# Performance work log

Hardware: AMD Instinct MI355X
Metric: run time of the kernel (lower is better)

Reference implementation:

```python
import jax, jax.numpy as jnp
import numpy as np
from jax import lax

KERNEL = 2  # kernel_size, forced by the (s3-1, s4-1, s5-1) output reshape


def setup_inputs() -> dict:
    key = jax.random.key(0)
    kx, kw = jax.random.split(key)
    x = jax.random.normal(kx, (4, 16, 32, 32, 32), dtype=jnp.float32)
    w = jax.random.normal(kw, (512, 128), dtype=jnp.float32)  # (d1, d2=C*2^3)
    return {"x": x, "w": w}


def _gaussian_kernel(x, w):
    N, C, D, H, W = x.shape
    d1, d2 = w.shape
    # 3D unfold with kernel 2, stride 1, no padding -> (N, C*8, D-1, H-1, W-1)
    patches = lax.conv_general_dilated_patches(
        x,
        filter_shape=(KERNEL, KERNEL, KERNEL),
        window_strides=(1, 1, 1),
        padding='VALID',
    )
    P = (D - 1) * (H - 1) * (W - 1)
    y = patches.reshape(N, d2, P).transpose(0, 2, 1)  # (N, P, d2)
    # sum((y - w)^2) expanded as ||y||^2 - 2 y.w + ||w||^2 to avoid the
    # (N, P, d1, d2) broadcasted difference tensor.
    y_sq = jnp.sum(y * y, axis=-1, keepdims=True)           # (N, P, 1)
    w_sq = jnp.sum(w * w, axis=-1)                          # (d1,)
    cross = jnp.einsum('npd,kd->npk', y, w)                 # (N, P, d1)
    dist = y_sq - 2.0 * cross + w_sq                        # (N, P, d1)
    out = jnp.exp(-dist)
    return out.transpose(0, 2, 1).reshape(N, d1, D - 1, H - 1, W - 1)


def reference(x, w):
    return _gaussian_kernel(x, w)
```

## Files before the change

kernel.cpp:

```cpp
#include <hip/hip_runtime.h>

typedef unsigned char u8;
typedef float f32x4 __attribute__((ext_vector_type(4)));

#define P_OUT 29791
#define NCH   512

__device__ __forceinline__ unsigned pk4_fp8(float a, float b, float c, float d) {
  int v = __builtin_amdgcn_cvt_pk_fp8_f32(a, b, 0, false);
  v = __builtin_amdgcn_cvt_pk_fp8_f32(c, d, v, true);
  return (unsigned)v;
}

__global__ void wprep_kernel(const float* __restrict__ w,
                             u8* __restrict__ wb, float* __restrict__ wsq) {
  const int tid = threadIdx.x;
  const int g = blockIdx.x * 16 + (tid >> 4);
  const int c = tid & 15;
  const float4* wr = (const float4*)(w + g * 128 + c * 8);
  float4 f0 = wr[0], f1 = wr[1];
  float s = f0.x*f0.x + f0.y*f0.y + f0.z*f0.z + f0.w*f0.w
          + f1.x*f1.x + f1.y*f1.y + f1.z*f1.z + f1.w*f1.w;
#pragma unroll
  for (int m = 1; m < 16; m <<= 1) s += __shfl_xor(s, m, 64);
  uint2 pk;
  pk.x = pk4_fp8(f0.x, f0.y, f0.z, f0.w);
  pk.y = pk4_fp8(f1.x, f1.y, f1.z, f1.w);
  *(uint2*)(wb + g * 128 + c * 8) = pk;
  if (c == 0) wsq[g] = s;
}

#define GLDS(g, l) __builtin_amdgcn_global_load_lds(                         \
    (const __attribute__((address_space(1))) unsigned int*)(g),              \
    (__attribute__((address_space(3))) unsigned int*)(l), 16, 0, 0)

__global__ __launch_bounds__(256, 2)
void gauss_fused_kernel(const float* __restrict__ x,
                        const u8* __restrict__ wb,
                        const float* __restrict__ wsq,
                        float* __restrict__ out) {
  __shared__ __align__(16) u8 Ws[128 * 128];
  __shared__ __align__(16) float Xs[16 * 2 * 5 * 32];

  const int bid = blockIdx.x;
  const int tile = (bid & 7) * 496 + (bid >> 3);
  const unsigned nb = (unsigned)tile / 992u;
  const unsigned rem = (unsigned)tile - nb * 992u;
  const unsigned ct = rem / 248u;
  const unsigned r2 = rem - ct * 248u;
  const unsigned d  = r2 >> 3;
  const unsigned hb = r2 & 7;
  const int h0 = hb * 4;
  const int nh = (h0 + 4 <= 31) ? 4 : (31 - h0);
  const int nrows = nh * 31;
  const int c0 = ct * 128;
  const int tp0 = d * 961 + h0 * 31;

  const int tid = threadIdx.x;
  const int wid = tid >> 6;
  const int lane = tid & 63;
  const int quad = lane >> 4;
  const int col = lane & 15;
  const int wch = wid & 1;
  const int wp = wid >> 1;

#pragma unroll
  for (int t = 0; t < 4; ++t) {
    const int Lb = (wid * 4 + t) * 64;
    const int L = Lb + lane;
    const int row = L >> 3;
    const int jc = (L & 7) ^ (row & 7);
    GLDS(wb + (size_t)(c0 + row) * 128 + jc * 16, &Ws[Lb * 16]);
  }

#pragma unroll
  for (int t = 0; t < 5; ++t) {
    const int Lb = t * 256 + wid * 64;
    const int L = Lb + lane;
    const int row = L >> 3;
    const int jc = L & 7;
    const unsigned c = (unsigned)row / 10u;
    const unsigned rr = (unsigned)row - c * 10u;
    const unsigned kd = rr / 5u;
    const unsigned hq = rr - kd * 5u;
    const int hg = h0 + (int)hq;
    const int hcl = (hg < 31) ? hg : 31;
    GLDS(x + (((size_t)(nb * 16 + c)) << 15) + (d + kd) * 1024 + hcl * 32 + jc * 4,
         &Xs[Lb * 4]);
  }

  int rb[4];
  int xoff[4];
#pragma unroll
  for (int j = 0; j < 4; ++j) {
    rb[j] = wp * 64 + j * 16 + col;
    const unsigned rc = (unsigned)((rb[j] < nrows) ? rb[j] : (nrows - 1));
    const unsigned hh = rc / 31u;
    const unsigned wv = rc - hh * 31u;
    xoff[j] = (int)(hh * 32 + wv);
  }

  f32x4 acc[4][4];
#pragma unroll
  for (int i = 0; i < 4; ++i)
#pragma unroll
    for (int j = 0; j < 4; ++j) acc[i][j] = (f32x4){0.f, 0.f, 0.f, 0.f};

  float sq[4] = {0.f, 0.f, 0.f, 0.f};

  __syncthreads();

  const int c16b = quad >> 1;
  const int hoff = (quad & 1) * 8;
#pragma unroll
  for (int ks = 0; ks < 4; ++ks) {
    long long a[4], b[4];
#pragma unroll
    for (int i = 0; i < 4; ++i) {
      const int rowA = wch * 64 + i * 16 + col;
      const int pa = (ks * 2 + c16b) ^ (rowA & 7);
      a[i] = *(const long long*)&Ws[rowA * 128 + pa * 16 + hoff];
    }
    const int cc = ks * 4 + quad;
    const float* xb = &Xs[cc * 320];
#pragma unroll
    for (int j = 0; j < 4; ++j) {
      const float* pB = xb + xoff[j];
      const float v0 = pB[0],   v1 = pB[1],   v2 = pB[32],  v3 = pB[33];
      const float v4 = pB[160], v5 = pB[161], v6 = pB[192], v7 = pB[193];
      sq[j] += v0*v0 + v1*v1 + v2*v2 + v3*v3 + v4*v4 + v5*v5 + v6*v6 + v7*v7;
      const unsigned lo = pk4_fp8(v0, v1, v2, v3);
      const unsigned hi = pk4_fp8(v4, v5, v6, v7);
      b[j] = (long long)(((unsigned long long)hi << 32) | lo);
    }
#pragma unroll
    for (int i = 0; i < 4; ++i)
#pragma unroll
      for (int j = 0; j < 4; ++j)
        acc[i][j] = __builtin_amdgcn_mfma_f32_16x16x32_fp8_fp8(a[i], b[j],
                                                               acc[i][j], 0, 0, 0);
  }

#pragma unroll
  for (int j = 0; j < 4; ++j) {
    sq[j] += __shfl_xor(sq[j], 16, 64);
    sq[j] += __shfl_xor(sq[j], 32, 64);
  }

  int pj[4];
#pragma unroll
  for (int j = 0; j < 4; ++j) pj[j] = tp0 + rb[j];

#pragma unroll
  for (int i = 0; i < 4; ++i) {
#pragma unroll
    for (int r = 0; r < 4; ++r) {
      const int ch = c0 + wch * 64 + i * 16 + quad * 4 + r;
      const float wsv = wsq[ch];
      float* ob = out + ((size_t)(nb * NCH + ch)) * P_OUT;
#pragma unroll
      for (int j = 0; j < 4; ++j)
        if (rb[j] < nrows)
          ob[pj[j]] = __expf(2.f * acc[i][j][r] - sq[j] - wsv);
    }
  }
}

extern "C" void kernel_launch(void* const* d_in, const int* in_sizes, int n_in,
                              void* d_out, int out_size, void* d_ws, size_t ws_size,
                              hipStream_t stream) {
  const float* x = (const float*)d_in[0];
  const float* w = (const float*)d_in[1];
  float* out = (float*)d_out;
  char* ws = (char*)d_ws;
  u8* wb     = (u8*)ws;
  float* wsq = (float*)(ws + 65536);

  wprep_kernel<<<32, 256, 0, stream>>>(w, wb, wsq);
  gauss_fused_kernel<<<3968, 256, 0, stream>>>(x, wb, wsq, out);
}
```

Baseline: 268.7 us.

## Stage fp8 patch tile in LDS once and raise occupancy target

The block now builds the unfolded patch operand cooperatively: each thread converts one patch row and half the channels to fp8 and writes it to a swizzled LDS buffer, along with per-row partial squared norms. Before, the waves that share patch columns each repeated that conversion and the squared-norm sum. The MFMA loop then reads B fragments from LDS just as it reads the weights. This adds an extra barrier and about 17KB more LDS per block, and the launch-bounds minimum goes from 2 to 3 blocks per CU, which limits registers.

```diff
diff --git a/kernel.cpp b/kernel.cpp
--- a/kernel.cpp
+++ b/kernel.cpp
@@ -34,13 +34,15 @@
     (const __attribute__((address_space(1))) unsigned int*)(g),              \
     (__attribute__((address_space(3))) unsigned int*)(l), 16, 0, 0)
 
-__global__ __launch_bounds__(256, 2)
+__global__ __launch_bounds__(256, 3)
 void gauss_fused_kernel(const float* __restrict__ x,
                         const u8* __restrict__ wb,
                         const float* __restrict__ wsq,
                         float* __restrict__ out) {
   __shared__ __align__(16) u8 Ws[128 * 128];
-  __shared__ __align__(16) float Xs[16 * 2 * 5 * 32];
+  __shared__ __align__(16) float Xs[5120];
+  __shared__ __align__(16) u8 Ys[128 * 128];
+  __shared__ float Yq[2][128];
 
   const int bid = blockIdx.x;
   const int tile = (bid & 7) * 496 + (bid >> 3);
@@ -89,16 +91,11 @@
          &Xs[Lb * 4]);
   }
 
-  int rb[4];
-  int xoff[4];
-#pragma unroll
-  for (int j = 0; j < 4; ++j) {
-    rb[j] = wp * 64 + j * 16 + col;
-    const unsigned rc = (unsigned)((rb[j] < nrows) ? rb[j] : (nrows - 1));
-    const unsigned hh = rc / 31u;
-    const unsigned wv = rc - hh * 31u;
-    xoff[j] = (int)(hh * 32 + wv);
-  }
+  const int prow = tid & 127;
+  const int pbh = tid >> 7;
+  const unsigned hh2 = (unsigned)prow / 31u;
+  const unsigned wv2 = (unsigned)prow - hh2 * 31u;
+  const int xo = (int)(hh2 * 32 + wv2);
 
   f32x4 acc[4][4];
 #pragma unroll
@@ -106,7 +103,26 @@
 #pragma unroll
     for (int j = 0; j < 4; ++j) acc[i][j] = (f32x4){0.f, 0.f, 0.f, 0.f};
 
-  float sq[4] = {0.f, 0.f, 0.f, 0.f};
+  __syncthreads();
+
+  if (prow < nrows) {
+    float sqp = 0.f;
+    const int wbase = prow * 128 + pbh * 8;
+    const int rsw = prow & 7;
+#pragma unroll
+    for (int it = 0; it < 8; ++it) {
+      const int c = it * 2 + pbh;
+      const float* pB = &Xs[c * 320 + xo];
+      const float v0 = pB[0],   v1 = pB[1],   v2 = pB[32],  v3 = pB[33];
+      const float v4 = pB[160], v5 = pB[161], v6 = pB[192], v7 = pB[193];
+      sqp += v0*v0 + v1*v1 + v2*v2 + v3*v3 + v4*v4 + v5*v5 + v6*v6 + v7*v7;
+      uint2 pk;
+      pk.x = pk4_fp8(v0, v1, v2, v3);
+      pk.y = pk4_fp8(v4, v5, v6, v7);
+      *(uint2*)&Ys[wbase + ((it ^ rsw) << 4)] = pk;
+    }
+    Yq[pbh][prow] = sqp;
+  }
 
   __syncthreads();
 
@@ -120,18 +136,9 @@
       const int rowA = wch * 64 + i * 16 + col;
       const int pa = (ks * 2 + c16b) ^ (rowA & 7);
       a[i] = *(const long long*)&Ws[rowA * 128 + pa * 16 + hoff];
-    }
-    const int cc = ks * 4 + quad;
-    const float* xb = &Xs[cc * 320];
-#pragma unroll
-    for (int j = 0; j < 4; ++j) {
-      const float* pB = xb + xoff[j];
-      const float v0 = pB[0],   v1 = pB[1],   v2 = pB[32],  v3 = pB[33];
-      const float v4 = pB[160], v5 = pB[161], v6 = pB[192], v7 = pB[193];
-      sq[j] += v0*v0 + v1*v1 + v2*v2 + v3*v3 + v4*v4 + v5*v5 + v6*v6 + v7*v7;
-      const unsigned lo = pk4_fp8(v0, v1, v2, v3);
-      const unsigned hi = pk4_fp8(v4, v5, v6, v7);
-      b[j] = (long long)(((unsigned long long)hi << 32) | lo);
+      const int rowB = wp * 64 + i * 16 + col;
+      const int pb = (ks * 2 + c16b) ^ (rowB & 7);
+      b[i] = *(const long long*)&Ys[rowB * 128 + pb * 16 + hoff];
     }
 #pragma unroll
     for (int i = 0; i < 4; ++i)
@@ -141,16 +148,14 @@
                                                                acc[i][j], 0, 0, 0);
   }
 
+  int rb[4];
+  float ysv[4];
 #pragma unroll
   for (int j = 0; j < 4; ++j) {
-    sq[j] += __shfl_xor(sq[j], 16, 64);
-    sq[j] += __shfl_xor(sq[j], 32, 64);
+    rb[j] = wp * 64 + j * 16 + col;
+    const int rc = (rb[j] < 124) ? rb[j] : 123;
+    ysv[j] = Yq[0][rc] + Yq[1][rc];
   }
-
-  int pj[4];
-#pragma unroll
-  for (int j = 0; j < 4; ++j) pj[j] = tp0 + rb[j];
-
 #pragma unroll
   for (int i = 0; i < 4; ++i) {
 #pragma unroll
@@ -161,7 +166,7 @@
 #pragma unroll
       for (int j = 0; j < 4; ++j)
         if (rb[j] < nrows)
-          ob[pj[j]] = __expf(2.f * acc[i][j][r] - sq[j] - wsv);
+          ob[tp0 + rb[j]] = __expf(2.f * acc[i][j][r] - ysv[j] - wsv);
     }
   }
 }
```

After: 298.2 us. 11.0% more time.

## Process all channel tiles per block with double-buffered fp8 weight tiles

Applied to the files above, without the earlier changes.

Each block now covers all four 128-channel weight tiles for its spatial tile, instead of one tile per block. The fp8-packed input patch fragments and their squared norms are computed once and kept in registers, where before every channel tile recomputed them. Weight tiles stream through two LDS buffers, and the next tile is loaded asynchronously while the current one is used. The grid shrinks fourfold, which reduces redundant x loads and conversions but lowers block-level parallelism and raises register pressure from holding the B fragments for all four k-steps.

```diff
diff --git a/kernel.cpp b/kernel.cpp
--- a/kernel.cpp
+++ b/kernel.cpp
@@ -39,21 +39,18 @@
                         const u8* __restrict__ wb,
                         const float* __restrict__ wsq,
                         float* __restrict__ out) {
-  __shared__ __align__(16) u8 Ws[128 * 128];
-  __shared__ __align__(16) float Xs[16 * 2 * 5 * 32];
+  __shared__ __align__(16) u8 Ws[2][128 * 128];
+  __shared__ __align__(16) float Xs[5120];
 
   const int bid = blockIdx.x;
-  const int tile = (bid & 7) * 496 + (bid >> 3);
-  const unsigned nb = (unsigned)tile / 992u;
-  const unsigned rem = (unsigned)tile - nb * 992u;
-  const unsigned ct = rem / 248u;
-  const unsigned r2 = rem - ct * 248u;
+  const int tile = (bid & 7) * 124 + (bid >> 3);
+  const unsigned nb = (unsigned)tile / 248u;
+  const unsigned r2 = (unsigned)tile - nb * 248u;
   const unsigned d  = r2 >> 3;
   const unsigned hb = r2 & 7;
   const int h0 = hb * 4;
   const int nh = (h0 + 4 <= 31) ? 4 : (31 - h0);
   const int nrows = nh * 31;
-  const int c0 = ct * 128;
   const int tp0 = d * 961 + h0 * 31;
 
   const int tid = threadIdx.x;
@@ -70,7 +67,7 @@
     const int L = Lb + lane;
     const int row = L >> 3;
     const int jc = (L & 7) ^ (row & 7);
-    GLDS(wb + (size_t)(c0 + row) * 128 + jc * 16, &Ws[Lb * 16]);
+    GLDS(wb + (size_t)row * 128 + jc * 16, &Ws[0][Lb * 16]);
   }
 
 #pragma unroll
@@ -100,27 +97,21 @@
     xoff[j] = (int)(hh * 32 + wv);
   }
 
-  f32x4 acc[4][4];
-#pragma unroll
-  for (int i = 0; i < 4; ++i)
-#pragma unroll
-    for (int j = 0; j < 4; ++j) acc[i][j] = (f32x4){0.f, 0.f, 0.f, 0.f};
-
+  __syncthreads();
+
+#pragma unroll
+  for (int t = 0; t < 4; ++t) {
+    const int Lb = (wid * 4 + t) * 64;
+    const int L = Lb + lane;
+    const int row = L >> 3;
+    const int jc = (L & 7) ^ (row & 7);
+    GLDS(wb + (size_t)(128 + row) * 128 + jc * 16, &Ws[1][Lb * 16]);
+  }
+
+  long long B[4][4];
   float sq[4] = {0.f, 0.f, 0.f, 0.f};
-
-  __syncthreads();
-
-  const int c16b = quad >> 1;
-  const int hoff = (quad & 1) * 8;
 #pragma unroll
   for (int ks = 0; ks < 4; ++ks) {
-    long long a[4], b[4];
-#pragma unroll
-    for (int i = 0; i < 4; ++i) {
-      const int rowA = wch * 64 + i * 16 + col;
-      const int pa = (ks * 2 + c16b) ^ (rowA & 7);
-      a[i] = *(const long long*)&Ws[rowA * 128 + pa * 16 + hoff];
-    }
     const int cc = ks * 4 + quad;
     const float* xb = &Xs[cc * 320];
 #pragma unroll
@@ -131,37 +122,74 @@
       sq[j] += v0*v0 + v1*v1 + v2*v2 + v3*v3 + v4*v4 + v5*v5 + v6*v6 + v7*v7;
       const unsigned lo = pk4_fp8(v0, v1, v2, v3);
       const unsigned hi = pk4_fp8(v4, v5, v6, v7);
-      b[j] = (long long)(((unsigned long long)hi << 32) | lo);
-    }
-#pragma unroll
-    for (int i = 0; i < 4; ++i)
-#pragma unroll
-      for (int j = 0; j < 4; ++j)
-        acc[i][j] = __builtin_amdgcn_mfma_f32_16x16x32_fp8_fp8(a[i], b[j],
-                                                               acc[i][j], 0, 0, 0);
-  }
-
+      B[ks][j] = (long long)(((unsigned long long)hi << 32) | lo);
+    }
+  }
 #pragma unroll
   for (int j = 0; j < 4; ++j) {
     sq[j] += __shfl_xor(sq[j], 16, 64);
     sq[j] += __shfl_xor(sq[j], 32, 64);
   }
 
-  int pj[4];
-#pragma unroll
-  for (int j = 0; j < 4; ++j) pj[j] = tp0 + rb[j];
-
-#pragma unroll
-  for (int i = 0; i < 4; ++i) {
-#pragma unroll
-    for (int r = 0; r < 4; ++r) {
-      const int ch = c0 + wch * 64 + i * 16 + quad * 4 + r;
-      const float wsv = wsq[ch];
-      float* ob = out + ((size_t)(nb * NCH + ch)) * P_OUT;
-#pragma unroll
-      for (int j = 0; j < 4; ++j)
-        if (rb[j] < nrows)
-          ob[pj[j]] = __expf(2.f * acc[i][j][r] - sq[j] - wsv);
+  const int c16b = quad >> 1;
+  const int hoff = (quad & 1) * 8;
+
+#pragma unroll
+  for (int ctit = 0; ctit < 4; ++ctit) {
+    const u8* Wcur = Ws[ctit & 1];
+
+    f32x4 acc[4][4];
+#pragma unroll
+    for (int i = 0; i < 4; ++i)
+#pragma unroll
+      for (int j = 0; j < 4; ++j) acc[i][j] = (f32x4){0.f, 0.f, 0.f, 0.f};
+
+#pragma unroll
+    for (int ks = 0; ks < 4; ++ks) {
+      long long a[4];
+#pragma unroll
+      for (int i = 0; i < 4; ++i) {
+        const int rowA = wch * 64 + i * 16 + col;
+        const int pa = (ks * 2 + c16b) ^ (rowA & 7);
+        a[i] = *(const long long*)&Wcur[rowA * 128 + pa * 16 + hoff];
+      }
+#pragma unroll
+      for (int i = 0; i < 4; ++i)
+#pragma unroll
+        for (int j = 0; j < 4; ++j)
+          acc[i][j] = __builtin_amdgcn_mfma_f32_16x16x32_fp8_fp8(a[i], B[ks][j],
+                                                                 acc[i][j], 0, 0, 0);
+    }
+
+    const int c0 = ctit * 128;
+#pragma unroll
+    for (int i = 0; i < 4; ++i) {
+#pragma unroll
+      for (int r = 0; r < 4; ++r) {
+        const int ch = c0 + wch * 64 + i * 16 + quad * 4 + r;
+        const float wsv = wsq[ch];
+        float* ob = out + ((size_t)(nb * NCH + ch)) * P_OUT;
+#pragma unroll
+        for (int j = 0; j < 4; ++j)
+          if (rb[j] < nrows)
+            ob[tp0 + rb[j]] = __expf(2.f * acc[i][j][r] - sq[j] - wsv);
+      }
+    }
+
+    if (ctit < 3) {
+      __syncthreads();
+      if (ctit < 2) {
+        u8* Wnext = Ws[ctit & 1];
+        const int ctn = ctit + 2;
+#pragma unroll
+        for (int t = 0; t < 4; ++t) {
+          const int Lb = (wid * 4 + t) * 64;
+          const int L = Lb + lane;
+          const int row = L >> 3;
+          const int jc = (L & 7) ^ (row & 7);
+          GLDS(wb + (size_t)(ctn * 128 + row) * 128 + jc * 16, &Wnext[Lb * 16]);
+        }
+      }
     }
   }
 }
@@ -177,5 +205,5 @@
   float* wsq = (float*)(ws + 65536);
 
   wprep_kernel<<<32, 256, 0, stream>>>(w, wb, wsq);
-  gauss_fused_kernel<<<3968, 256, 0, stream>>>(x, wb, wsq, out);
-}
+  gauss_fused_kernel<<<992, 256, 0, stream>>>(x, wb, wsq, out);
+}
```

Result: slower. 278.9 us (+3.8%).

## Double spatial tile per block to 512 threads with 8-row h tiles

Applied to the files above, without the earlier changes.

Each block now handles 8 h-rows (248 positions) instead of 4, using 512 threads and 1984 blocks. The X halo staging grows to 9 h-rows per depth slice, so the overlapping halo is loaded less often relative to useful rows. The W tile load is split across twice as many waves. B operands for all k-steps are now built into registers before the MFMA loop. The larger block raises register and LDS use per block, which may reduce occupancy.

```diff
diff --git a/kernel.cpp b/kernel.cpp
--- a/kernel.cpp
+++ b/kernel.cpp
@@ -34,27 +34,27 @@
     (const __attribute__((address_space(1))) unsigned int*)(g),              \
     (__attribute__((address_space(3))) unsigned int*)(l), 16, 0, 0)
 
-__global__ __launch_bounds__(256, 2)
+__global__ __launch_bounds__(512)
 void gauss_fused_kernel(const float* __restrict__ x,
                         const u8* __restrict__ wb,
                         const float* __restrict__ wsq,
                         float* __restrict__ out) {
   __shared__ __align__(16) u8 Ws[128 * 128];
-  __shared__ __align__(16) float Xs[16 * 2 * 5 * 32];
+  __shared__ __align__(16) float Xs[9216];
 
   const int bid = blockIdx.x;
-  const int tile = (bid & 7) * 496 + (bid >> 3);
-  const unsigned nb = (unsigned)tile / 992u;
-  const unsigned rem = (unsigned)tile - nb * 992u;
-  const unsigned ct = rem / 248u;
-  const unsigned r2 = rem - ct * 248u;
-  const unsigned d  = r2 >> 3;
-  const unsigned hb = r2 & 7;
-  const int h0 = hb * 4;
-  const int nh = (h0 + 4 <= 31) ? 4 : (31 - h0);
-  const int nrows = nh * 31;
+  const int tile = (bid & 7) * 248 + (bid >> 3);
+  const unsigned pq = (unsigned)tile & 3u;
+  const unsigned t2 = (unsigned)tile >> 2;
+  const unsigned d  = t2 % 31u;
+  const unsigned t3 = t2 / 31u;
+  const unsigned ct = t3 & 3u;
+  const unsigned nb = t3 >> 2;
+
+  const int h0 = pq * 8;
+  const int nrows = (pq < 3) ? 248 : 217;
+  const int tp0 = d * 961 + pq * 248;
   const int c0 = ct * 128;
-  const int tp0 = d * 961 + h0 * 31;
 
   const int tid = threadIdx.x;
   const int wid = tid >> 6;
@@ -65,8 +65,8 @@
   const int wp = wid >> 1;
 
 #pragma unroll
-  for (int t = 0; t < 4; ++t) {
-    const int Lb = (wid * 4 + t) * 64;
+  for (int t = 0; t < 2; ++t) {
+    const int Lb = (wid * 2 + t) * 64;
     const int L = Lb + lane;
     const int row = L >> 3;
     const int jc = (L & 7) ^ (row & 7);
@@ -75,18 +75,20 @@
 
 #pragma unroll
   for (int t = 0; t < 5; ++t) {
-    const int Lb = t * 256 + wid * 64;
-    const int L = Lb + lane;
-    const int row = L >> 3;
-    const int jc = L & 7;
-    const unsigned c = (unsigned)row / 10u;
-    const unsigned rr = (unsigned)row - c * 10u;
-    const unsigned kd = rr / 5u;
-    const unsigned hq = rr - kd * 5u;
-    const int hg = h0 + (int)hq;
-    const int hcl = (hg < 31) ? hg : 31;
-    GLDS(x + (((size_t)(nb * 16 + c)) << 15) + (d + kd) * 1024 + hcl * 32 + jc * 4,
-         &Xs[Lb * 4]);
+    if (t < 4 || wid < 4) {
+      const int Lb = t * 512 + wid * 64;
+      const int L = Lb + lane;
+      const int row = L >> 3;
+      const int jc = L & 7;
+      const unsigned c = (unsigned)row / 18u;
+      const unsigned rr = (unsigned)row - c * 18u;
+      const unsigned kd = rr / 9u;
+      const unsigned hq = rr - kd * 9u;
+      const int hg = h0 + (int)hq;
+      const int hcl = (hg < 31) ? hg : 31;
+      GLDS(x + (((size_t)(nb * 16 + c)) << 15) + (d + kd) * 1024 + hcl * 32 + jc * 4,
+           &Xs[Lb * 4]);
+    }
   }
 
   int rb[4];
@@ -100,56 +102,55 @@
     xoff[j] = (int)(hh * 32 + wv);
   }
 
+  __syncthreads();
+
+  long long B[4][4];
+  float sq[4] = {0.f, 0.f, 0.f, 0.f};
+#pragma unroll
+  for (int ks = 0; ks < 4; ++ks) {
+    const int cc = ks * 4 + quad;
+    const float* xb = &Xs[cc * 576];
+#pragma unroll
+    for (int j = 0; j < 4; ++j) {
+      const float* pB = xb + xoff[j];
+      const float v0 = pB[0],   v1 = pB[1],   v2 = pB[32],  v3 = pB[33];
+      const float v4 = pB[288], v5 = pB[289], v6 = pB[320], v7 = pB[321];
+      sq[j] += v0*v0 + v1*v1 + v2*v2 + v3*v3 + v4*v4 + v5*v5 + v6*v6 + v7*v7;
+      const unsigned lo = pk4_fp8(v0, v1, v2, v3);
+      const unsigned hi = pk4_fp8(v4, v5, v6, v7);
+      B[ks][j] = (long long)(((unsigned long long)hi << 32) | lo);
+    }
+  }
+#pragma unroll
+  for (int j = 0; j < 4; ++j) {
+    sq[j] += __shfl_xor(sq[j], 16, 64);
+    sq[j] += __shfl_xor(sq[j], 32, 64);
+  }
+
   f32x4 acc[4][4];
 #pragma unroll
   for (int i = 0; i < 4; ++i)
 #pragma unroll
     for (int j = 0; j < 4; ++j) acc[i][j] = (f32x4){0.f, 0.f, 0.f, 0.f};
 
-  float sq[4] = {0.f, 0.f, 0.f, 0.f};
-
-  __syncthreads();
-
   const int c16b = quad >> 1;
   const int hoff = (quad & 1) * 8;
 #pragma unroll
   for (int ks = 0; ks < 4; ++ks) {
-    long long a[4], b[4];
+    long long a[4];
 #pragma unroll
     for (int i = 0; i < 4; ++i) {
       const int rowA = wch * 64 + i * 16 + col;
       const int pa = (ks * 2 + c16b) ^ (rowA & 7);
       a[i] = *(const long long*)&Ws[rowA * 128 + pa * 16 + hoff];
     }
-    const int cc = ks * 4 + quad;
-    const float* xb = &Xs[cc * 320];
-#pragma unroll
-    for (int j = 0; j < 4; ++j) {
-      const float* pB = xb + xoff[j];
-      const float v0 = pB[0],   v1 = pB[1],   v2 = pB[32],  v3 = pB[33];
-      const float v4 = pB[160], v5 = pB[161], v6 = pB[192], v7 = pB[193];
-      sq[j] += v0*v0 + v1*v1 + v2*v2 + v3*v3 + v4*v4 + v5*v5 + v6*v6 + v7*v7;
-      const unsigned lo = pk4_fp8(v0, v1, v2, v3);
-      const unsigned hi = pk4_fp8(v4, v5, v6, v7);
-      b[j] = (long long)(((unsigned long long)hi << 32) | lo);
-    }
 #pragma unroll
     for (int i = 0; i < 4; ++i)
 #pragma unroll
       for (int j = 0; j < 4; ++j)
-        acc[i][j] = __builtin_amdgcn_mfma_f32_16x16x32_fp8_fp8(a[i], b[j],
+        acc[i][j] = __builtin_amdgcn_mfma_f32_16x16x32_fp8_fp8(a[i], B[ks][j],
                                                                acc[i][j], 0, 0, 0);
   }
-
-#pragma unroll
-  for (int j = 0; j < 4; ++j) {
-    sq[j] += __shfl_xor(sq[j], 16, 64);
-    sq[j] += __shfl_xor(sq[j], 32, 64);
-  }
-
-  int pj[4];
-#pragma unroll
-  for (int j = 0; j < 4; ++j) pj[j] = tp0 + rb[j];
 
 #pragma unroll
   for (int i = 0; i < 4; ++i) {
@@ -161,7 +162,7 @@
 #pragma unroll
       for (int j = 0; j < 4; ++j)
         if (rb[j] < nrows)
-          ob[pj[j]] = __expf(2.f * acc[i][j][r] - sq[j] - wsv);
+          ob[tp0 + rb[j]] = __expf(2.f * acc[i][j][r] - sq[j] - wsv);
     }
   }
 }
@@ -177,5 +178,5 @@
   float* wsq = (float*)(ws + 65536);
 
   wprep_kernel<<<32, 256, 0, stream>>>(w, wb, wsq);
-  gauss_fused_kernel<<<3968, 256, 0, stream>>>(x, wb, wsq, out);
+  gauss_fused_kernel<<<1984, 512, 0, stream>>>(x, wb, wsq, out);
 }
```

Measured after the change: 298.0 us. 1.11x slower.
